# Optimization experiments

Hardware: AMD Instinct MI355X
Metric: run time of the kernel (lower is better)

## Reference

```python
import jax, jax.numpy as jnp
import numpy as np

C = 1024
H = 16
DH = C // H
DFF = 4 * C
D = 1024  # cond_dim
B = 2
L = 2048
MAX_SCALE_MUL = float(np.log(100.0))
EPS = 1e-6


def _ln(x):
    # LayerNorm without affine, eps=1e-6
    m = jnp.mean(x, axis=-1, keepdims=True)
    xc = x - m
    var = jnp.mean(xc * xc, axis=-1, keepdims=True)
    return xc * jax.lax.rsqrt(var + EPS)


def setup_inputs() -> dict:
    key = jax.random.key(0)
    ks = jax.random.split(key, 16)
    s = 0.02
    return {
        "x": jax.random.normal(ks[0], (B, L, C), jnp.float32),
        "cond_BD": jax.random.normal(ks[1], (B, D), jnp.float32),
        "attn_bias": jax.random.normal(ks[2], (1, 1, L, L), jnp.float32) * 0.1,
        "qkv_w": jax.random.normal(ks[3], (3 * C, C), jnp.float32) * s,
        "q_bias": jnp.zeros((C,), jnp.float32),
        "v_bias": jnp.zeros((C,), jnp.float32),
        "scale_mul": jnp.full((1, H, 1, 1), np.log(4.0), jnp.float32),
        "proj_w": jax.random.normal(ks[4], (C, C), jnp.float32) * s,
        "proj_b": jnp.zeros((C,), jnp.float32),
        "fc1_w": jax.random.normal(ks[5], (DFF, C), jnp.float32) * s,
        "fc1_b": jnp.zeros((DFF,), jnp.float32),
        "fc2_w": jax.random.normal(ks[6], (C, DFF), jnp.float32) * s,
        "fc2_b": jnp.zeros((C,), jnp.float32),
        "ada_w": jax.random.normal(ks[7], (6 * C, D), jnp.float32) * s,
        "ada_b": jnp.zeros((6 * C,), jnp.float32),
    }


def _attention(x, attn_bias, qkv_w, q_bias, v_bias, scale_mul, proj_w, proj_b):
    b, l, c = x.shape
    bias = jnp.concatenate([q_bias, jnp.zeros_like(q_bias), v_bias])
    qkv = x @ qkv_w.T + bias  # [B,L,3C]
    qkv = qkv.reshape(b, l, 3, H, DH).transpose(2, 0, 3, 1, 4)  # [3,B,H,L,DH]
    q, k, v = qkv[0], qkv[1], qkv[2]
    sm = jnp.exp(jnp.minimum(scale_mul, MAX_SCALE_MUL))  # [1,H,1,1]
    q = q * jax.lax.rsqrt(jnp.sum(q * q, -1, keepdims=True).clip(1e-24)) * sm
    k = k * jax.lax.rsqrt(jnp.sum(k * k, -1, keepdims=True).clip(1e-24))
    attn = jnp.einsum("bhqd,bhkd->bhqk", q, k) + attn_bias
    attn = jax.nn.softmax(attn, axis=-1)
    out = jnp.einsum("bhqk,bhkd->bhqd", attn, v)
    out = out.transpose(0, 2, 1, 3).reshape(b, l, c)
    return out @ proj_w.T + proj_b


def reference(x, cond_BD, attn_bias, qkv_w, q_bias, v_bias, scale_mul,
              proj_w, proj_b, fc1_w, fc1_b, fc2_w, fc2_b, ada_w, ada_b):
    # adaLN modulation: SiLU -> Linear -> 6 chunks of C
    ada = jax.nn.silu(cond_BD) @ ada_w.T + ada_b  # [B,6C]
    ada = ada.reshape(-1, 1, 6, C)
    g1, g2, s1, s2, sh1, sh2 = [ada[:, :, i, :] for i in range(6)]  # each [B,1,C]
    # attention branch
    h = _ln(x) * (s1 + 1.0) + sh1
    x = x + _attention(h, attn_bias, qkv_w, q_bias, v_bias, scale_mul, proj_w, proj_b) * g1
    # FFN branch (GELU tanh approx)
    h = _ln(x) * (s2 + 1.0) + sh2
    h = jax.nn.gelu(h @ fc1_w.T + fc1_b, approximate=True) @ fc2_w.T + fc2_b
    x = x + h * g2
    return x
```

## Files before the change

kernel.cpp:

```cpp
#include <hip/hip_runtime.h>
#include <stdint.h>

#define Ll 2048
#define Mrows 4096
#define LOG2E 1.44269504088896f

typedef unsigned short u16;
typedef __attribute__((ext_vector_type(8))) short short8;
typedef __attribute__((ext_vector_type(4))) float f32x4;

#if __has_builtin(__builtin_amdgcn_exp2f)
#define EXP2F(x) __builtin_amdgcn_exp2f(x)
#else
#define EXP2F(x) exp2f(x)
#endif

__device__ __forceinline__ float b2f(u16 b) {
  union { float f; unsigned u; } x; x.u = ((unsigned)b) << 16; return x.f;
}
__device__ __forceinline__ u16 f2b(float v) {
  union { float f; unsigned u; } x; x.f = v;
  unsigned r = x.u + 0x7fffu + ((x.u >> 16) & 1u);
  return (u16)(r >> 16);
}

#define GLOAD_LDS16(gp, sp)                                                        \
  __builtin_amdgcn_global_load_lds(                                                \
      (__attribute__((address_space(1))) void*)(void*)(gp),                        \
      (__attribute__((address_space(3))) void*)(sp), 16, 0, 0)

__global__ __launch_bounds__(256) void k_convert_all(
    const float* __restrict__ s0, u16* __restrict__ d0,
    const float* __restrict__ s1, u16* __restrict__ d1,
    const float* __restrict__ s2, u16* __restrict__ d2,
    const float* __restrict__ s3, u16* __restrict__ d3,
    const float* __restrict__ s4, float* __restrict__ d4) {
  int i = blockIdx.x * 256 + threadIdx.x;
  if (i >= 3145728) {
    i -= 3145728;
    float4 v = ((const float4*)s4)[i];
    v.x *= LOG2E; v.y *= LOG2E; v.z *= LOG2E; v.w *= LOG2E;
    ((float4*)d4)[i] = v;
    return;
  }
  const float* s; u16* d; int off;
  if (i < 786432)       { s = s0; d = d0; off = 0; }
  else if (i < 1048576) { s = s1; d = d1; off = 786432; }
  else if (i < 2097152) { s = s2; d = d2; off = 1048576; }
  else                  { s = s3; d = d3; off = 2097152; }
  i -= off;
  const float4 v = ((const float4*)s)[i];
  ushort4 o;
  o.x = f2b(v.x); o.y = f2b(v.y); o.z = f2b(v.z); o.w = f2b(v.w);
  ((ushort4*)d)[i] = o;
}

__global__ __launch_bounds__(256) void k_ada(const float* __restrict__ cond,
                                             const float* __restrict__ aw,
                                             const float* __restrict__ ab,
                                             float* __restrict__ out) {
  const int wv = threadIdx.x >> 6, lane = threadIdx.x & 63;
  const int j = blockIdx.x * 4 + wv;
  const int b = j / 6144, jj = j % 6144;
  const float* wr = aw + (size_t)jj * 1024;
  const float* cr = cond + b * 1024;
  float acc = 0.f;
  for (int d = lane; d < 1024; d += 64) {
    const float cv = cr[d];
    acc += (cv / (1.f + __expf(-cv))) * wr[d];
  }
  for (int off = 32; off; off >>= 1) acc += __shfl_xor(acc, off);
  if (lane == 0) out[b * 6144 + jj] = acc + ab[jj];
}

__global__ __launch_bounds__(256) void k_ln_mod(const float* __restrict__ x,
                                                const float* __restrict__ ada,
                                                u16* __restrict__ out,
                                                int s_off, int sh_off) {
  const int row = blockIdx.x;
  const int b = row >> 11;
  const int t = threadIdx.x;
  const float4 xv = ((const float4*)(x + (size_t)row * 1024))[t];
  float s = xv.x + xv.y + xv.z + xv.w;
  float s2 = xv.x * xv.x + xv.y * xv.y + xv.z * xv.z + xv.w * xv.w;
  for (int off = 32; off; off >>= 1) { s += __shfl_xor(s, off); s2 += __shfl_xor(s2, off); }
  __shared__ float red[8];
  const int wv = t >> 6, lane = t & 63;
  if (lane == 0) { red[wv] = s; red[4 + wv] = s2; }
  __syncthreads();
  s = red[0] + red[1] + red[2] + red[3];
  s2 = red[4] + red[5] + red[6] + red[7];
  const float mean = s * (1.f / 1024.f);
  const float var = s2 * (1.f / 1024.f) - mean * mean;
  const float rstd = rsqrtf(var + 1e-6f);
  const float4 sv = ((const float4*)(ada + b * 6144 + s_off))[t];
  const float4 shv = ((const float4*)(ada + b * 6144 + sh_off))[t];
  ushort4 ov;
  ov.x = f2b((xv.x - mean) * rstd * (1.f + sv.x) + shv.x);
  ov.y = f2b((xv.y - mean) * rstd * (1.f + sv.y) + shv.y);
  ov.z = f2b((xv.z - mean) * rstd * (1.f + sv.z) + shv.z);
  ov.w = f2b((xv.w - mean) * rstd * (1.f + sv.w) + shv.w);
  ((ushort4*)(out + (size_t)row * 1024))[t] = ov;
}

__global__ __launch_bounds__(256) void k_resid_ln(const float* __restrict__ x,
                                                  const float* __restrict__ p0,
                                                  const float* __restrict__ p1,
                                                  const float* __restrict__ ada,
                                                  float* __restrict__ x2,
                                                  u16* __restrict__ out) {
  const int row = blockIdx.x;
  const int b = row >> 11;
  const int t = threadIdx.x;
  const float4 xv = ((const float4*)(x + (size_t)row * 1024))[t];
  const float4 pa = ((const float4*)(p0 + (size_t)row * 1024))[t];
  const float4 pb = ((const float4*)(p1 + (size_t)row * 1024))[t];
  const float4 gv = ((const float4*)(ada + b * 6144 + 0))[t];
  float4 v;
  v.x = xv.x + (pa.x + pb.x) * gv.x; v.y = xv.y + (pa.y + pb.y) * gv.y;
  v.z = xv.z + (pa.z + pb.z) * gv.z; v.w = xv.w + (pa.w + pb.w) * gv.w;
  ((float4*)(x2 + (size_t)row * 1024))[t] = v;
  float s = v.x + v.y + v.z + v.w;
  float s2 = v.x * v.x + v.y * v.y + v.z * v.z + v.w * v.w;
  for (int off = 32; off; off >>= 1) { s += __shfl_xor(s, off); s2 += __shfl_xor(s2, off); }
  __shared__ float red[8];
  const int wv = t >> 6, lane = t & 63;
  if (lane == 0) { red[wv] = s; red[4 + wv] = s2; }
  __syncthreads();
  s = red[0] + red[1] + red[2] + red[3];
  s2 = red[4] + red[5] + red[6] + red[7];
  const float mean = s * (1.f / 1024.f);
  const float var = s2 * (1.f / 1024.f) - mean * mean;
  const float rstd = rsqrtf(var + 1e-6f);
  const float4 sv = ((const float4*)(ada + b * 6144 + 3072))[t];
  const float4 shv = ((const float4*)(ada + b * 6144 + 5120))[t];
  ushort4 ov;
  ov.x = f2b((v.x - mean) * rstd * (1.f + sv.x) + shv.x);
  ov.y = f2b((v.y - mean) * rstd * (1.f + sv.y) + shv.y);
  ov.z = f2b((v.z - mean) * rstd * (1.f + sv.z) + shv.z);
  ov.w = f2b((v.w - mean) * rstd * (1.f + sv.w) + shv.w);
  ((ushort4*)(out + (size_t)row * 1024))[t] = ov;
}

__global__ __launch_bounds__(256) void k_final(const float* __restrict__ x2,
                                               const float* __restrict__ f0,
                                               const float* __restrict__ f1,
                                               const float* __restrict__ ada,
                                               float* __restrict__ out) {
  const int i = blockIdx.x * 256 + threadIdx.x;
  const int elem = i * 4;
  const int b = elem >> 21;
  const int c = elem & 1023;
  const float4 xv = ((const float4*)x2)[i];
  const float4 fa = ((const float4*)f0)[i];
  const float4 fb = ((const float4*)f1)[i];
  const float4 gv = *(const float4*)(ada + b * 6144 + 1024 + c);
  float4 ov;
  ov.x = xv.x + (fa.x + fb.x) * gv.x; ov.y = xv.y + (fa.y + fb.y) * gv.y;
  ov.z = xv.z + (fa.z + fb.z) * gv.z; ov.w = xv.w + (fa.w + fb.w) * gv.w;
  ((float4*)out)[i] = ov;
}

template <int OUT_BF16, int GELU_ACT>
__global__ __launch_bounds__(256, 2)
void k_gemm_bt(const u16* __restrict__ A, const u16* __restrict__ W,
               const float* __restrict__ bias, void* __restrict__ Cout,
               float* __restrict__ Cout2, int M, int N, int Kc) {
  __shared__ u16 As[128 * 64];
  __shared__ u16 Bs[128 * 64];
  const int tid = threadIdx.x;
  const int wv = tid >> 6;
  const int lane = tid & 63;
  const int q = lane >> 4;
  const int r = lane & 15;
  const int wm = (wv & 1) * 64;
  const int wn = (wv >> 1) * 64;
  const int m0 = blockIdx.x * 128;
  const int n0 = blockIdx.y * 128;
  const int K = Kc * gridDim.z;
  const int kt0 = blockIdx.z * Kc;

  f32x4 acc[4][4];
#pragma unroll
  for (int i = 0; i < 4; ++i)
#pragma unroll
    for (int j = 0; j < 4; ++j) acc[i][j] = (f32x4)0.0f;

  const int srow = tid >> 3;
  const int scol = (tid & 7) * 8;
  const u16* Ag = A + (size_t)(m0 + srow) * K + scol;
  const u16* Wg = W + (size_t)(n0 + srow) * K + scol;
  u16* AsBase = &As[wv * 512];
  u16* BsBase = &Bs[wv * 512];

  for (int kt = kt0; kt < kt0 + Kc; kt += 64) {
    __syncthreads();
#pragma unroll
    for (int p = 0; p < 4; ++p) {
      GLOAD_LDS16(Ag + (size_t)(p * 32) * K + kt, AsBase + p * 2048);
      GLOAD_LDS16(Wg + (size_t)(p * 32) * K + kt, BsBase + p * 2048);
    }
    __syncthreads();
#pragma unroll
    for (int kc = 0; kc < 2; ++kc) {
      short8 af[4], bfr[4];
#pragma unroll
      for (int i = 0; i < 4; ++i) {
        af[i] = *(const short8*)(As + (wm + i * 16 + r) * 64 + kc * 32 + q * 8);
        bfr[i] = *(const short8*)(Bs + (wn + i * 16 + r) * 64 + kc * 32 + q * 8);
      }
#pragma unroll
      for (int mi = 0; mi < 4; ++mi)
#pragma unroll
        for (int ni = 0; ni < 4; ++ni)
          acc[mi][ni] = __builtin_amdgcn_mfma_f32_16x16x32_bf16(af[mi], bfr[ni],
                                                                acc[mi][ni], 0, 0, 0);
    }
  }
  float* Cf = (blockIdx.z == 0) ? (float*)Cout : Cout2;
#pragma unroll
  for (int mi = 0; mi < 4; ++mi) {
#pragma unroll
    for (int ni = 0; ni < 4; ++ni) {
      const int col = n0 + wn + ni * 16 + r;
      const float bv = (blockIdx.z == 0) ? bias[col] : 0.f;
#pragma unroll
      for (int rr = 0; rr < 4; ++rr) {
        const int rowg = m0 + wm + mi * 16 + q * 4 + rr;
        float v = acc[mi][ni][rr] + bv;
        if (GELU_ACT) {
          const float t = tanhf(0.7978845608028654f * (v + 0.044715f * v * v * v));
          v = 0.5f * v * (1.0f + t);
        }
        if (OUT_BF16)
          ((u16*)Cout)[(size_t)rowg * N + col] = f2b(v);
        else
          Cf[(size_t)rowg * N + col] = v;
      }
    }
  }
}

__global__ __launch_bounds__(256, 2)
void k_gemm_qkv(const u16* __restrict__ A, const u16* __restrict__ W,
                const float* __restrict__ qb, const float* __restrict__ vb,
                const float* __restrict__ scale_mul, u16* __restrict__ Cout) {
  const int N = 3072, K = 1024;
  __shared__ u16 As[128 * 64];
  __shared__ u16 Bs[128 * 64];
  const int tid = threadIdx.x;
  const int wv = tid >> 6;
  const int lane = tid & 63;
  const int q = lane >> 4;
  const int r = lane & 15;
  const int wm = (wv & 1) * 64;
  const int wn = (wv >> 1) * 64;
  const int m0 = blockIdx.x * 128;
  const int n0 = blockIdx.y * 128;

  f32x4 acc[4][4];
#pragma unroll
  for (int i = 0; i < 4; ++i)
#pragma unroll
    for (int j = 0; j < 4; ++j) acc[i][j] = (f32x4)0.0f;

  const int srow = tid >> 3;
  const int scol = (tid & 7) * 8;
  const u16* Ag = A + (size_t)(m0 + srow) * K + scol;
  const u16* Wg = W + (size_t)(n0 + srow) * K + scol;
  u16* AsBase = &As[wv * 512];
  u16* BsBase = &Bs[wv * 512];

  for (int kt = 0; kt < K; kt += 64) {
    __syncthreads();
#pragma unroll
    for (int p = 0; p < 4; ++p) {
      GLOAD_LDS16(Ag + (size_t)(p * 32) * K + kt, AsBase + p * 2048);
      GLOAD_LDS16(Wg + (size_t)(p * 32) * K + kt, BsBase + p * 2048);
    }
    __syncthreads();
#pragma unroll
    for (int kc = 0; kc < 2; ++kc) {
      short8 af[4], bfr[4];
#pragma unroll
      for (int i = 0; i < 4; ++i) {
        af[i] = *(const short8*)(As + (wm + i * 16 + r) * 64 + kc * 32 + q * 8);
        bfr[i] = *(const short8*)(Bs + (wn + i * 16 + r) * 64 + kc * 32 + q * 8);
      }
#pragma unroll
      for (int mi = 0; mi < 4; ++mi)
#pragma unroll
        for (int ni = 0; ni < 4; ++ni)
          acc[mi][ni] = __builtin_amdgcn_mfma_f32_16x16x32_bf16(af[mi], bfr[ni],
                                                                acc[mi][ni], 0, 0, 0);
    }
  }
  const int cb = n0 + wn;
  const int sec = cb >> 10;
  const int hh = (cb >> 6) & 15;
  const float sm = (sec == 0)
      ? __expf(fminf(scale_mul[hh], 4.605170185988091f)) * LOG2E : 1.f;
#pragma unroll
  for (int mi = 0; mi < 4; ++mi) {
    float v[4][4];
#pragma unroll
    for (int ni = 0; ni < 4; ++ni) {
      const int d = ni * 16 + r;
      const float bvv = (sec == 0) ? qb[(cb & 1023) + d]
                        : (sec == 2 ? vb[(cb & 1023) + d] : 0.f);
#pragma unroll
      for (int rr = 0; rr < 4; ++rr) v[ni][rr] = acc[mi][ni][rr] + bvv;
    }
    if (sec < 2) {
#pragma unroll
      for (int rr = 0; rr < 4; ++rr) {
        float ss = v[0][rr] * v[0][rr] + v[1][rr] * v[1][rr] +
                   v[2][rr] * v[2][rr] + v[3][rr] * v[3][rr];
        ss += __shfl_xor(ss, 1); ss += __shfl_xor(ss, 2);
        ss += __shfl_xor(ss, 4); ss += __shfl_xor(ss, 8);
        const float sc = rsqrtf(fmaxf(ss, 1e-24f)) * sm;
#pragma unroll
        for (int ni = 0; ni < 4; ++ni) v[ni][rr] *= sc;
      }
    }
#pragma unroll
    for (int ni = 0; ni < 4; ++ni) {
      const int col = cb + ni * 16 + r;
#pragma unroll
      for (int rr = 0; rr < 4; ++rr) {
        const int rowg = m0 + wm + mi * 16 + q * 4 + rr;
        Cout[(size_t)rowg * N + col] = f2b(v[ni][rr]);
      }
    }
  }
}

__global__ __launch_bounds__(512)
void k_flash(const u16* __restrict__ qkv, const float* __restrict__ bl2e,
             u16* __restrict__ o) {
  __shared__ u16 Qs[128 * 64];
  __shared__ u16 Ks[64 * 64];
  __shared__ u16 Vt[64 * 72];
  __shared__ u16 Ps[8][16 * 72];
  __shared__ float stat[8][16];
  const int tid = threadIdx.x;
  const int bh = blockIdx.x;
  const int qb = blockIdx.y;
  const int b = bh >> 4, h = bh & 15;
  const int wv = tid >> 6, lane = tid & 63;
  const int quad = lane >> 4, c = lane & 15;
  const u16* Qg = qkv + (size_t)b * Ll * 3072 + h * 64;
  const u16* Kg = Qg + 1024;
  const u16* Vg = Qg + 2048;
  const int srow = tid >> 3, scol = (tid & 7) * 8;

  {
    const u16* gp = Qg + (size_t)(qb * 128 + srow) * 3072 + scol;
    GLOAD_LDS16(gp, &Qs[wv * 512]);
    GLOAD_LDS16(gp + (size_t)64 * 3072, &Qs[4096 + wv * 512]);
  }
  const int vc = tid & 15, va = (tid >> 4) & 1, vd0 = (tid >> 5) * 4;

  f32x4 O[4];
  float lacc[4];
#pragma unroll
  for (int i = 0; i < 4; ++i) { O[i] = (f32x4)0.f; lacc[i] = 0.f; }
  const float* bb = bl2e + (size_t)(qb * 128 + wv * 16 + quad * 4) * 2048 + c;

  for (int kt = 0; kt < 32; ++kt) {
    __syncthreads();
    GLOAD_LDS16(Kg + (size_t)(kt * 64 + srow) * 3072 + scol, &Ks[wv * 512]);
    {
      const u16* vp = Vg + (size_t)(kt * 64 + va * 32 + vc) * 3072 + vd0;
      const ushort4 r0 = *(const ushort4*)vp;
      const ushort4 r1 = *(const ushort4*)(vp + (size_t)16 * 3072);
      u16* vt = &Vt[vd0 * 72 + vc * 4 + va * 2];
      *(unsigned*)(vt + 0 * 72) = (unsigned)r0.x | ((unsigned)r1.x << 16);
      *(unsigned*)(vt + 1 * 72) = (unsigned)r0.y | ((unsigned)r1.y << 16);
      *(unsigned*)(vt + 2 * 72) = (unsigned)r0.z | ((unsigned)r1.z << 16);
      *(unsigned*)(vt + 3 * 72) = (unsigned)r0.w | ((unsigned)r1.w << 16);
    }
    __syncthreads();

    f32x4 S[4];
#pragma unroll
    for (int ni = 0; ni < 4; ++ni)
#pragma unroll
      for (int rr = 0; rr < 4; ++rr)
        S[ni][rr] = bb[rr * 2048 + kt * 64 + ni * 16];
#pragma unroll
    for (int ks = 0; ks < 2; ++ks) {
      const short8 aq = *(const short8*)(&Qs[(wv * 16 + c) * 64 + ks * 32 + quad * 8]);
#pragma unroll
      for (int ni = 0; ni < 4; ++ni) {
        const short8 bk = *(const short8*)(&Ks[(ni * 16 + c) * 64 + ks * 32 + quad * 8]);
        S[ni] = __builtin_amdgcn_mfma_f32_16x16x32_bf16(aq, bk, S[ni], 0, 0, 0);
      }
    }

#pragma unroll
    for (int rr = 0; rr < 4; ++rr) {
      union { float f; unsigned u; } p0, p1, p2, p3;
      p0.f = EXP2F(S[0][rr]); p1.f = EXP2F(S[1][rr]);
      p2.f = EXP2F(S[2][rr]); p3.f = EXP2F(S[3][rr]);
      lacc[rr] += (p0.f + p1.f) + (p2.f + p3.f);
      uint2 pk;
      pk.x = __builtin_amdgcn_perm(p1.u + 0x8000u, p0.u + 0x8000u, 0x07060302u);
      pk.y = __builtin_amdgcn_perm(p3.u + 0x8000u, p2.u + 0x8000u, 0x07060302u);
      *(uint2*)(&Ps[wv][(quad * 4 + rr) * 72 + c * 4]) = pk;
    }
    __threadfence_block();
#pragma unroll
    for (int ks = 0; ks < 2; ++ks) {
      const short8 bp = *(const short8*)(&Ps[wv][c * 72 + ks * 32 + quad * 8]);
#pragma unroll
      for (int i = 0; i < 4; ++i) {
        const short8 av = *(const short8*)(&Vt[(i * 16 + c) * 72 + ks * 32 + quad * 8]);
        O[i] = __builtin_amdgcn_mfma_f32_16x16x32_bf16(av, bp, O[i], 0, 0, 0);
      }
    }
  }

#pragma unroll
  for (int rr = 0; rr < 4; ++rr) {
    float l = lacc[rr];
    l += __shfl_xor(l, 1); l += __shfl_xor(l, 2);
    l += __shfl_xor(l, 4); l += __shfl_xor(l, 8);
    lacc[rr] = l;
  }
  if (c == 0)
    *(float4*)(&stat[wv][quad * 4]) = make_float4(lacc[0], lacc[1], lacc[2], lacc[3]);
  __threadfence_block();
  const float inv = 1.f / stat[wv][c];
  u16* op = o + (size_t)(b * Ll + qb * 128 + wv * 16 + c) * 1024 + h * 64;
#pragma unroll
  for (int i = 0; i < 4; ++i) {
    ushort4 ov;
    ov.x = f2b(O[i][0] * inv); ov.y = f2b(O[i][1] * inv);
    ov.z = f2b(O[i][2] * inv); ov.w = f2b(O[i][3] * inv);
    *(ushort4*)(op + i * 16 + quad * 4) = ov;
  }
}

extern "C" void kernel_launch(void* const* d_in, const int* in_sizes, int n_in,
                              void* d_out, int out_size, void* d_ws, size_t ws_size,
                              hipStream_t stream) {
  const float* x = (const float*)d_in[0];
  const float* cond = (const float*)d_in[1];
  const float* attn_bias = (const float*)d_in[2];
  const float* qkv_w = (const float*)d_in[3];
  const float* q_bias = (const float*)d_in[4];
  const float* v_bias = (const float*)d_in[5];
  const float* scale_mul = (const float*)d_in[6];
  const float* proj_w = (const float*)d_in[7];
  const float* proj_b = (const float*)d_in[8];
  const float* fc1_w = (const float*)d_in[9];
  const float* fc1_b = (const float*)d_in[10];
  const float* fc2_w = (const float*)d_in[11];
  const float* fc2_b = (const float*)d_in[12];
  const float* ada_w = (const float*)d_in[13];
  const float* ada_b = (const float*)d_in[14];
  float* out = (float*)d_out;
  char* ws = (char*)d_ws;

  float* ada_out = (float*)(ws + 0);
  u16* wqkv = (u16*)(ws + 61440);
  u16* wproj = (u16*)(ws + 6352896);
  u16* wfc1 = (u16*)(ws + 8450048);
  u16* wfc2 = (u16*)(ws + 16838656);
  u16* sb = (u16*)(ws + 25227264);
  u16* big = (u16*)(ws + 33615872);
  float* g32 = (float*)(ws + 67170304);
  float* x2 = (float*)(ws + 83947520);
  float* bl2e = x2;
  float* projp0 = (float*)big;
  float* projp1 = (float*)(big + (size_t)8 * 1024 * 1024);
  float* fc2p1 = (float*)(ws + 61440);

  k_convert_all<<<16384, 256, 0, stream>>>(qkv_w, wqkv, proj_w, wproj,
                                           fc1_w, wfc1, fc2_w, wfc2,
                                           attn_bias, bl2e);
  k_ada<<<3072, 256, 0, stream>>>(cond, ada_w, ada_b, ada_out);
  k_ln_mod<<<4096, 256, 0, stream>>>(x, ada_out, sb, 2048, 4096);
  k_gemm_qkv<<<dim3(32, 24), 256, 0, stream>>>(sb, wqkv, q_bias, v_bias,
                                               scale_mul, big);
  k_flash<<<dim3(32, 16), 512, 0, stream>>>(big, bl2e, sb);
  k_gemm_bt<0, 0><<<dim3(32, 8, 2), 256, 0, stream>>>(sb, wproj, proj_b, projp0,
                                                      projp1, Mrows, 1024, 512);
  k_resid_ln<<<4096, 256, 0, stream>>>(x, projp0, projp1, ada_out, x2, sb);
  k_gemm_bt<1, 1><<<dim3(32, 32, 1), 256, 0, stream>>>(sb, wfc1, fc1_b, big,
                                                       nullptr, Mrows, 4096, 1024);
  k_gemm_bt<0, 0><<<dim3(32, 8, 2), 256, 0, stream>>>(big, wfc2, fc2_b, g32,
                                                      fc2p1, Mrows, 1024, 2048);
  k_final<<<4096, 256, 0, stream>>>(x2, g32, fc2p1, ada_out, out);
}
```

Before: 446.3 us.

## Double-buffer K/V tiles and prefetch bias in flash attention loop

The flash attention kernel now uses two LDS buffers for K and transposed V. While the current tile is being computed, it issues the K, V and bias loads for the next tile, which also lets it drop one of the two barriers per iteration. The aim is to hide global-memory latency behind the MFMA and softmax work. The cost is more LDS per block and more registers for the prefetched bias and V values, which could lower occupancy.

```diff
diff --git a/kernel.cpp b/kernel.cpp
--- a/kernel.cpp
+++ b/kernel.cpp
@@ -339,8 +339,8 @@
 void k_flash(const u16* __restrict__ qkv, const float* __restrict__ bl2e,
              u16* __restrict__ o) {
   __shared__ u16 Qs[128 * 64];
-  __shared__ u16 Ks[64 * 64];
-  __shared__ u16 Vt[64 * 72];
+  __shared__ u16 Ks[2][64 * 64];
+  __shared__ u16 Vt[2][64 * 72];
   __shared__ u16 Ps[8][16 * 72];
   __shared__ float stat[8][16];
   const int tid = threadIdx.x;
@@ -353,13 +353,13 @@
   const u16* Kg = Qg + 1024;
   const u16* Vg = Qg + 2048;
   const int srow = tid >> 3, scol = (tid & 7) * 8;
+  const int vc = tid & 15, va = (tid >> 4) & 1, vd0 = (tid >> 5) * 4;
 
   {
     const u16* gp = Qg + (size_t)(qb * 128 + srow) * 3072 + scol;
     GLOAD_LDS16(gp, &Qs[wv * 512]);
     GLOAD_LDS16(gp + (size_t)64 * 3072, &Qs[4096 + wv * 512]);
   }
-  const int vc = tid & 15, va = (tid >> 4) & 1, vd0 = (tid >> 5) * 4;
 
   f32x4 O[4];
   float lacc[4];
@@ -367,37 +367,53 @@
   for (int i = 0; i < 4; ++i) { O[i] = (f32x4)0.f; lacc[i] = 0.f; }
   const float* bb = bl2e + (size_t)(qb * 128 + wv * 16 + quad * 4) * 2048 + c;
 
-  for (int kt = 0; kt < 32; ++kt) {
+  float bA[4][4], bB[4][4];
+  GLOAD_LDS16(Kg + (size_t)srow * 3072 + scol, &Ks[0][wv * 512]);
+  {
+    const u16* vp = Vg + (size_t)(va * 32 + vc) * 3072 + vd0;
+    const ushort4 r0 = *(const ushort4*)vp;
+    const ushort4 r1 = *(const ushort4*)(vp + (size_t)16 * 3072);
+    u16* vt = &Vt[0][vd0 * 72 + vc * 4 + va * 2];
+    *(unsigned*)(vt + 0 * 72) = (unsigned)r0.x | ((unsigned)r1.x << 16);
+    *(unsigned*)(vt + 1 * 72) = (unsigned)r0.y | ((unsigned)r1.y << 16);
+    *(unsigned*)(vt + 2 * 72) = (unsigned)r0.z | ((unsigned)r1.z << 16);
+    *(unsigned*)(vt + 3 * 72) = (unsigned)r0.w | ((unsigned)r1.w << 16);
+  }
+#pragma unroll
+  for (int ni = 0; ni < 4; ++ni)
+#pragma unroll
+    for (int rr = 0; rr < 4; ++rr) bA[ni][rr] = bb[rr * 2048 + ni * 16];
+
+  auto tile = [&](int kt, u16* KsC, u16* KsN, u16* VtC, u16* VtN,
+                  float (&bC)[4][4], float (&bN)[4][4]) __attribute__((always_inline)) {
+    const int ktn = (kt < 31) ? kt + 1 : 31;
     __syncthreads();
-    GLOAD_LDS16(Kg + (size_t)(kt * 64 + srow) * 3072 + scol, &Ks[wv * 512]);
+    GLOAD_LDS16(Kg + (size_t)(ktn * 64 + srow) * 3072 + scol, &KsN[wv * 512]);
+    ushort4 vr0, vr1;
     {
-      const u16* vp = Vg + (size_t)(kt * 64 + va * 32 + vc) * 3072 + vd0;
-      const ushort4 r0 = *(const ushort4*)vp;
-      const ushort4 r1 = *(const ushort4*)(vp + (size_t)16 * 3072);
-      u16* vt = &Vt[vd0 * 72 + vc * 4 + va * 2];
-      *(unsigned*)(vt + 0 * 72) = (unsigned)r0.x | ((unsigned)r1.x << 16);
-      *(unsigned*)(vt + 1 * 72) = (unsigned)r0.y | ((unsigned)r1.y << 16);
-      *(unsigned*)(vt + 2 * 72) = (unsigned)r0.z | ((unsigned)r1.z << 16);
-      *(unsigned*)(vt + 3 * 72) = (unsigned)r0.w | ((unsigned)r1.w << 16);
-    }
-    __syncthreads();
-
+      const u16* vp = Vg + (size_t)(ktn * 64 + va * 32 + vc) * 3072 + vd0;
+      vr0 = *(const ushort4*)vp;
+      vr1 = *(const ushort4*)(vp + (size_t)16 * 3072);
+    }
+#pragma unroll
+    for (int ni = 0; ni < 4; ++ni)
+#pragma unroll
+      for (int rr = 0; rr < 4; ++rr)
+        bN[ni][rr] = bb[rr * 2048 + ktn * 64 + ni * 16];
     f32x4 S[4];
 #pragma unroll
     for (int ni = 0; ni < 4; ++ni)
 #pragma unroll
-      for (int rr = 0; rr < 4; ++rr)
-        S[ni][rr] = bb[rr * 2048 + kt * 64 + ni * 16];
+      for (int rr = 0; rr < 4; ++rr) S[ni][rr] = bC[ni][rr];
 #pragma unroll
     for (int ks = 0; ks < 2; ++ks) {
       const short8 aq = *(const short8*)(&Qs[(wv * 16 + c) * 64 + ks * 32 + quad * 8]);
 #pragma unroll
       for (int ni = 0; ni < 4; ++ni) {
-        const short8 bk = *(const short8*)(&Ks[(ni * 16 + c) * 64 + ks * 32 + quad * 8]);
+        const short8 bk = *(const short8*)(&KsC[(ni * 16 + c) * 64 + ks * 32 + quad * 8]);
         S[ni] = __builtin_amdgcn_mfma_f32_16x16x32_bf16(aq, bk, S[ni], 0, 0, 0);
       }
     }
-
 #pragma unroll
     for (int rr = 0; rr < 4; ++rr) {
       union { float f; unsigned u; } p0, p1, p2, p3;
@@ -415,10 +431,22 @@
       const short8 bp = *(const short8*)(&Ps[wv][c * 72 + ks * 32 + quad * 8]);
 #pragma unroll
       for (int i = 0; i < 4; ++i) {
-        const short8 av = *(const short8*)(&Vt[(i * 16 + c) * 72 + ks * 32 + quad * 8]);
+        const short8 av = *(const short8*)(&VtC[(i * 16 + c) * 72 + ks * 32 + quad * 8]);
         O[i] = __builtin_amdgcn_mfma_f32_16x16x32_bf16(av, bp, O[i], 0, 0, 0);
       }
     }
+    {
+      u16* vt = &VtN[vd0 * 72 + vc * 4 + va * 2];
+      *(unsigned*)(vt + 0 * 72) = (unsigned)vr0.x | ((unsigned)vr1.x << 16);
+      *(unsigned*)(vt + 1 * 72) = (unsigned)vr0.y | ((unsigned)vr1.y << 16);
+      *(unsigned*)(vt + 2 * 72) = (unsigned)vr0.z | ((unsigned)vr1.z << 16);
+      *(unsigned*)(vt + 3 * 72) = (unsigned)vr0.w | ((unsigned)vr1.w << 16);
+    }
+  };
+
+  for (int kt = 0; kt < 32; kt += 2) {
+    tile(kt,     Ks[0], Ks[1], Vt[0], Vt[1], bA, bB);
+    tile(kt + 1, Ks[1], Ks[0], Vt[1], Vt[0], bB, bA);
   }
 
 #pragma unroll
```

New measurement: 432.9 us. 3.0% less time.
